# Kernel tuning notes

Hardware: AMD Instinct MI355X
Metric: run time of the kernel (lower is better)

Reference implementation:

```python
import jax, jax.numpy as jnp
import numpy as np
import math

NL = 2
ENC = 64

def _ln(x, g, b):
    m = x.mean(-1, keepdims=True)
    v = ((x - m) ** 2).mean(-1, keepdims=True)
    return (x - m) * jax.lax.rsqrt(v + 1e-5) * g + b

def _sinu(vals):
    half = ENC // 2
    freq = jnp.exp(jnp.arange(half, dtype=vals.dtype) * (-math.log(10000.0) / half))
    a = vals[..., None] * freq
    return jnp.concatenate([jnp.sin(a), jnp.cos(a)], -1)

def _ssm(x, ng, nb, piw, pib, pw, pb, ig, ib):
    # SSMBlock with LinearAttention core: x + proj_out(LN(silu(z)*sigmoid(gate)))
    h = _ln(x, ng, nb)
    zi = h @ piw + pib
    z, gate = jnp.split(zi, 2, axis=-1)
    u = _ln(jax.nn.silu(z) * jax.nn.sigmoid(gate), ig, ib)
    return x + u @ pw + pb

def _fwd(s, attn_maps, km, se_w1, se_b1, se_w2, se_b2,
         f_ng, f_nb, f_piw, f_pib, f_pow, f_pob, f_ig, f_ib,
         b_ng, b_nb, b_piw, b_pib, b_pow, b_pob, b_ig, b_ib,
         mrg_w, mrg_b, nrm_g, nrm_b,
         ffn_ng, ffn_nb, ffn_w1, ffn_b1, ffn_w2, ffn_b2, H, W):
    B, K, D = s.shape
    w = attn_maps / (attn_maps.sum(-1, keepdims=True) + 1e-8)  # [B,K,N]
    gy = jnp.arange(H, dtype=s.dtype) / max(H - 1, 1)
    gx = jnp.arange(W, dtype=s.dtype) / max(W - 1, 1)
    grid_y = jnp.repeat(gy, W)  # [N], meshgrid-ij flattened
    grid_x = jnp.tile(gx, H)
    cy = (w * grid_y).sum(-1)  # [B,K]
    cx = (w * grid_x).sum(-1)
    spread = jnp.sqrt((w * ((grid_y - cy[..., None]) ** 2 + (grid_x - cx[..., None]) ** 2)).sum(-1))
    enc = jnp.concatenate([_sinu(cy), _sinu(cx), spread[..., None]], -1)  # [B,K,129]
    s = s + jax.nn.gelu(enc @ se_w1 + se_b1, approximate=False) @ se_w2 + se_b2
    # spatial order: identical every layer since attn_maps is fixed
    order = jnp.argsort(cy * W + cx, axis=-1)  # [B,K]
    rv = jnp.argsort(order, axis=-1)           # inverse permutation
    for i in range(NL):
        r = s
        so = jnp.take_along_axis(s, order[..., None], axis=1)
        f = _ssm(so, f_ng[i], f_nb[i], f_piw[i], f_pib[i], f_pow[i], f_pob[i], f_ig[i], f_ib[i])
        bb = jnp.flip(_ssm(jnp.flip(so, 1), b_ng[i], b_nb[i], b_piw[i], b_pib[i], b_pow[i], b_pob[i], b_ig[i], b_ib[i]), 1)
        m = jnp.concatenate([f, bb], -1) @ mrg_w[i] + mrg_b[i]
        s = _ln(r + jnp.take_along_axis(m, rv[..., None], axis=1), nrm_g[i], nrm_b[i])
        h = _ln(s, ffn_ng[i], ffn_nb[i])
        s = s + jax.nn.gelu(h @ ffn_w1[i] + ffn_b1[i], approximate=False) @ ffn_w2[i] + ffn_b2[i]
        s = s * km[..., None]
    return s

def setup_inputs() -> dict:
    B, K, D, DI, H, W = 32, 256, 512, 1024, 64, 64
    N = H * W
    ks = iter(jax.random.split(jax.random.key(0), 64))
    def g(shape, sc=0.02):
        return jax.random.normal(next(ks), shape, dtype=jnp.float32) * sc
    inp = {
        's': jax.random.normal(next(ks), (B, K, D), dtype=jnp.float32),
        'attn_maps': jax.random.uniform(next(ks), (B, K, N), dtype=jnp.float32),
        'km': jnp.ones((B, K), jnp.float32),
        'se_w1': g((2 * ENC + 1, D)), 'se_b1': jnp.zeros((D,), jnp.float32),
        'se_w2': g((D, D)), 'se_b2': jnp.zeros((D,), jnp.float32),
    }
    for p in ('f', 'b'):
        inp[p + '_ng'] = jnp.ones((NL, D), jnp.float32)
        inp[p + '_nb'] = jnp.zeros((NL, D), jnp.float32)
        inp[p + '_piw'] = g((NL, D, 2 * DI))
        inp[p + '_pib'] = jnp.zeros((NL, 2 * DI), jnp.float32)
        inp[p + '_pow'] = g((NL, DI, D))
        inp[p + '_pob'] = jnp.zeros((NL, D), jnp.float32)
        inp[p + '_ig'] = jnp.ones((NL, DI), jnp.float32)
        inp[p + '_ib'] = jnp.zeros((NL, DI), jnp.float32)
    inp['mrg_w'] = g((NL, 2 * D, D)); inp['mrg_b'] = jnp.zeros((NL, D), jnp.float32)
    inp['nrm_g'] = jnp.ones((NL, D), jnp.float32); inp['nrm_b'] = jnp.zeros((NL, D), jnp.float32)
    inp['ffn_ng'] = jnp.ones((NL, D), jnp.float32); inp['ffn_nb'] = jnp.zeros((NL, D), jnp.float32)
    inp['ffn_w1'] = g((NL, D, 4 * D)); inp['ffn_b1'] = jnp.zeros((NL, 4 * D), jnp.float32)
    inp['ffn_w2'] = g((NL, 4 * D, D)); inp['ffn_b2'] = jnp.zeros((NL, D), jnp.float32)
    inp['H'] = H
    inp['W'] = W
    return inp

def reference(s, attn_maps, km, se_w1, se_b1, se_w2, se_b2,
              f_ng, f_nb, f_piw, f_pib, f_pow, f_pob, f_ig, f_ib,
              b_ng, b_nb, b_piw, b_pib, b_pow, b_pob, b_ig, b_ib,
              mrg_w, mrg_b, nrm_g, nrm_b,
              ffn_ng, ffn_nb, ffn_w1, ffn_b1, ffn_w2, ffn_b2, H, W):
    return _fwd(s, attn_maps, km, se_w1, se_b1, se_w2, se_b2,
                f_ng, f_nb, f_piw, f_pib, f_pow, f_pob, f_ig, f_ib,
                b_ng, b_nb, b_piw, b_pib, b_pow, b_pob, b_ig, b_ib,
                mrg_w, mrg_b, nrm_g, nrm_b,
                ffn_ng, ffn_nb, ffn_w1, ffn_b1, ffn_w2, ffn_b2, H, W)
```

## Files before the change

kernel.cpp:

```cpp
#include <hip/hip_runtime.h>
#include <cstdint>
#include <cstddef>


typedef unsigned short u16;
typedef __bf16 bf16x8 __attribute__((ext_vector_type(8)));
typedef float f32x4 __attribute__((ext_vector_type(4)));

#define MROWS 8192

__device__ __forceinline__ u16 f2bf(float f){
  unsigned u = __float_as_uint(f);
  u += 0x7FFFu + ((u >> 16) & 1u);
  return (u16)(u >> 16);
}
__device__ __forceinline__ float bf2f(u16 v){
  return __uint_as_float((unsigned)v << 16);
}

__device__ __forceinline__ float wred64(float v){
#pragma unroll
  for (int o = 32; o > 0; o >>= 1) v += __shfl_xor(v, o, 64);
  return v;
}

#define GLD16(gp, lp) __builtin_amdgcn_global_load_lds( \
    (const __attribute__((address_space(1))) unsigned int*)(gp), \
    (__attribute__((address_space(3))) unsigned int*)(lp), 16, 0, 0)

struct TDesc { const float* src; u16* dst; int R, Kpad, C, zgate, nbx, base; };
struct TPack { TDesc d[16]; };

__global__ __launch_bounds__(256) void transpose_all(TPack p){
  int bid = blockIdx.x;
  TDesc dd = p.d[0];
#pragma unroll
  for (int i = 1; i < 16; ++i) if (bid >= p.d[i].base) dd = p.d[i];
  int lb = bid - dd.base;
  int bx = lb % dd.nbx, by = lb / dd.nbx;

  __shared__ float tile[32][33];
  int n0 = bx << 5, k0 = by << 5;
  int tx = threadIdx.x & 31, ty = threadIdx.x >> 5;
#pragma unroll
  for (int i = 0; i < 32; i += 8){
    int k = k0 + ty + i, n = n0 + tx;
    int oc = n;
    if (dd.zgate){ int g = n >> 5, sl = n & 31;
      oc = (sl < 16) ? (g << 4) + sl : (dd.C >> 1) + (g << 4) + sl - 16; }
    tile[ty + i][tx] = (k < dd.R) ? dd.src[(size_t)k * dd.C + oc] : 0.f;
  }
  __syncthreads();
#pragma unroll
  for (int i = 0; i < 32; i += 8){
    int n = n0 + ty + i, k = k0 + tx;
    dd.dst[(size_t)n * dd.Kpad + k] = f2bf(tile[tx][ty + i]);
  }
}

__global__ __launch_bounds__(256) void stats_enc(
    const float* __restrict__ attn, u16* __restrict__ enc){
  int row = blockIdx.x;
  const float4* a4 = (const float4*)(attn + (size_t)row * 4096);
  int t = threadIdx.x;
  const float inv63 = 1.0f / 63.0f;
  float s0 = 0, sy = 0, sx = 0, sy2 = 0, sx2 = 0;
#pragma unroll
  for (int i = 0; i < 4; ++i){
    int c = t + 256 * i;
    float4 v = a4[c];
    int n = 4 * c;
#pragma unroll
    for (int e = 0; e < 4; ++e){
      float av = (&v.x)[e];
      int nn = n + e;
      float gy = (float)(nn >> 6) * inv63;
      float gx = (float)(nn & 63) * inv63;
      s0 += av; sy += av * gy; sx += av * gx;
      sy2 += av * gy * gy; sx2 += av * gx * gx;
    }
  }
  s0 = wred64(s0); sy = wred64(sy); sx = wred64(sx);
  sy2 = wred64(sy2); sx2 = wred64(sx2);
  __shared__ float red[4][5];
  __shared__ float outv[3];
  int wv = t >> 6, lane = t & 63;
  if (lane == 0){ red[wv][0]=s0; red[wv][1]=sy; red[wv][2]=sx; red[wv][3]=sy2; red[wv][4]=sx2; }
  __syncthreads();
  if (t == 0){
    float S=0, Ay=0, Ax=0, Ay2=0, Ax2=0;
    for (int w = 0; w < 4; ++w){ S+=red[w][0]; Ay+=red[w][1]; Ax+=red[w][2]; Ay2+=red[w][3]; Ax2+=red[w][4]; }
    float denom = S + 1e-8f;
    float cy = Ay / denom, cx = Ax / denom;
    float sp2 = (Ay2 - 2.f*cy*Ay + cy*cy*S + Ax2 - 2.f*cx*Ax + cx*cx*S) / denom;
    outv[0] = cy; outv[1] = cx; outv[2] = sqrtf(fmaxf(sp2, 0.f));
  }
  __syncthreads();
  if (t < 192){
    float cy = outv[0], cx = outv[1];
    float val = 0.f;
    if (t < 128){
      int j = t & 31;
      float fr = expf(-0.28782313662425572f * (float)j);
      float base = (t < 64) ? cy : cx;
      float ang = base * fr;
      val = ((t >> 5) & 1) ? cosf(ang) : sinf(ang);
    } else if (t == 128) val = outv[2];
    enc[(size_t)row * 192 + t] = f2bf(val);
  }
}

__global__ __launch_bounds__(256) void ln_dual(
    const float* __restrict__ x,
    const float* __restrict__ g1, const float* __restrict__ b1,
    const float* __restrict__ g2, const float* __restrict__ b2,
    u16* __restrict__ o1, u16* __restrict__ o2){
  int row = blockIdx.x * 4 + (threadIdx.x >> 6);
  int lane = threadIdx.x & 63, c = lane * 8;
  const float* xr = x + (size_t)row * 512 + c;
  float v[8];
  *(float4*)(v) = *(const float4*)(xr); *(float4*)(v+4) = *(const float4*)(xr+4);
  float s = 0.f;
#pragma unroll
  for (int j = 0; j < 8; ++j) s += v[j];
  float m = wred64(s) * (1.f/512.f);
  float q = 0.f;
#pragma unroll
  for (int j = 0; j < 8; ++j){ float d = v[j]-m; q += d*d; }
  float rstd = rsqrtf(wred64(q)*(1.f/512.f) + 1e-5f);
  float G1[8],B1[8],G2[8],B2[8];
  *(float4*)(G1)=*(const float4*)(g1+c); *(float4*)(G1+4)=*(const float4*)(g1+c+4);
  *(float4*)(B1)=*(const float4*)(b1+c); *(float4*)(B1+4)=*(const float4*)(b1+c+4);
  *(float4*)(G2)=*(const float4*)(g2+c); *(float4*)(G2+4)=*(const float4*)(g2+c+4);
  *(float4*)(B2)=*(const float4*)(b2+c); *(float4*)(B2+4)=*(const float4*)(b2+c+4);
  u16 u1[8] __attribute__((aligned(16)));
  u16 u2[8] __attribute__((aligned(16)));
#pragma unroll
  for (int j = 0; j < 8; ++j){
    float nv = (v[j]-m)*rstd;
    u1[j] = f2bf(nv*G1[j]+B1[j]);
    u2[j] = f2bf(nv*G2[j]+B2[j]);
  }
  *(uint4*)(o1 + (size_t)row*512 + c) = *(const uint4*)u1;
  *(uint4*)(o2 + (size_t)row*512 + c) = *(const uint4*)u2;
}

__global__ __launch_bounds__(256) void ln1024(
    const u16* __restrict__ x, const float* __restrict__ g,
    const float* __restrict__ b, u16* __restrict__ o){
  int row = blockIdx.x * 4 + (threadIdx.x >> 6);
  int lane = threadIdx.x & 63, c = lane * 16;
  const u16* xr = x + (size_t)row * 1024 + c;
  u16 raw[16] __attribute__((aligned(16)));
  *(uint4*)(raw)     = *(const uint4*)(xr);
  *(uint4*)(raw + 8) = *(const uint4*)(xr + 8);
  float v[16];
#pragma unroll
  for (int j = 0; j < 16; ++j) v[j] = bf2f(raw[j]);
  float s = 0.f;
#pragma unroll
  for (int j = 0; j < 16; ++j) s += v[j];
  float m = wred64(s) * (1.f/1024.f);
  float q = 0.f;
#pragma unroll
  for (int j = 0; j < 16; ++j){ float d = v[j]-m; q += d*d; }
  float rstd = rsqrtf(wred64(q)*(1.f/1024.f) + 1e-5f);
  float G[16], B[16];
#pragma unroll
  for (int i = 0; i < 4; ++i){
    *(float4*)(G + 4*i) = *(const float4*)(g + c + 4*i);
    *(float4*)(B + 4*i) = *(const float4*)(b + c + 4*i);
  }
  u16 u[16] __attribute__((aligned(16)));
#pragma unroll
  for (int j = 0; j < 16; ++j) u[j] = f2bf((v[j]-m)*rstd*G[j] + B[j]);
  *(uint4*)(o + (size_t)row*1024 + c)     = *(const uint4*)(u);
  *(uint4*)(o + (size_t)row*1024 + c + 8) = *(const uint4*)(u + 8);
}

__global__ __launch_bounds__(256) void ln_double(
    const float* __restrict__ x,
    const float* __restrict__ ng, const float* __restrict__ nb,
    const float* __restrict__ fg, const float* __restrict__ fbv,
    float* __restrict__ s1, u16* __restrict__ h2){
  int row = blockIdx.x * 4 + (threadIdx.x >> 6);
  int lane = threadIdx.x & 63, c = lane * 8;
  const float* xr = x + (size_t)row * 512 + c;
  float v[8];
  *(float4*)(v) = *(const float4*)(xr); *(float4*)(v+4) = *(const float4*)(xr+4);
  float s = 0.f;
#pragma unroll
  for (int j = 0; j < 8; ++j) s += v[j];
  float m = wred64(s) * (1.f/512.f);
  float q = 0.f;
#pragma unroll
  for (int j = 0; j < 8; ++j){ float d = v[j]-m; q += d*d; }
  float rstd = rsqrtf(wred64(q)*(1.f/512.f) + 1e-5f);
  float NG[8],NB[8],FG[8],FB[8];
  *(float4*)(NG)=*(const float4*)(ng+c); *(float4*)(NG+4)=*(const float4*)(ng+c+4);
  *(float4*)(NB)=*(const float4*)(nb+c); *(float4*)(NB+4)=*(const float4*)(nb+c+4);
  *(float4*)(FG)=*(const float4*)(fg+c); *(float4*)(FG+4)=*(const float4*)(fg+c+4);
  *(float4*)(FB)=*(const float4*)(fbv+c);*(float4*)(FB+4)=*(const float4*)(fbv+c+4);
  float w[8];
#pragma unroll
  for (int j = 0; j < 8; ++j) w[j] = (v[j]-m)*rstd*NG[j] + NB[j];
  *(float4*)(s1 + (size_t)row*512 + c)   = *(const float4*)(w);
  *(float4*)(s1 + (size_t)row*512 + c+4) = *(const float4*)(w+4);
  float s2 = 0.f;
#pragma unroll
  for (int j = 0; j < 8; ++j) s2 += w[j];
  float m2 = wred64(s2) * (1.f/512.f);
  float q2 = 0.f;
#pragma unroll
  for (int j = 0; j < 8; ++j){ float d = w[j]-m2; q2 += d*d; }
  float rstd2 = rsqrtf(wred64(q2)*(1.f/512.f) + 1e-5f);
  u16 u[8] __attribute__((aligned(16)));
#pragma unroll
  for (int j = 0; j < 8; ++j) u[j] = f2bf((w[j]-m2)*rstd2*FG[j] + FB[j]);
  *(uint4*)(h2 + (size_t)row*512 + c) = *(const uint4*)u;
}

template<int EPI, int BM>
__global__ __launch_bounds__(256, 2) void gemm_bt(
    const u16* __restrict__ A, const u16* __restrict__ BT,
    const float* __restrict__ bias, const float* __restrict__ res,
    float* __restrict__ outF, u16* __restrict__ outB,
    const float* __restrict__ km,
    int K, int N, int ldo, int coloff){
  constexpr int MR = BM / 32;
  __shared__ u16 Asm[BM * 64];
  __shared__ u16 Bsm[128 * 64];
  const int tid = threadIdx.x, wv = tid >> 6, lane = tid & 63;
  const int m0 = blockIdx.y * BM, n0 = blockIdx.x << 7;
  const int wr = wv >> 1, wc = wv & 1;

  const int rowin = lane >> 3;
  const int ksrc = ((16 * (lane & 7)) ^ (rowin << 4)) >> 1;
  const int rA = wv * (BM / 4) + rowin;
  const int rB = (wv << 5) + rowin;
  const u16* gA = A + (size_t)(m0 + rA) * K + ksrc;
  const u16* gB = BT + (size_t)(n0 + rB) * K + ksrc;
  u16* ldsA = Asm + wv * (BM / 4) * 64;
  u16* ldsB = Bsm + (wv << 11);

  f32x4 acc[MR][4] = {};
  const int cbase = 16 * (lane >> 4);
  const int swz = (lane & 7) << 4;

  for (int kt = 0; kt < K; kt += 64){
#pragma unroll
    for (int it = 0; it < BM / 32; ++it)
      GLD16(gA + (size_t)it * 8 * K + kt, ldsA + it * 512);
#pragma unroll
    for (int it = 0; it < 4; ++it)
      GLD16(gB + (size_t)it * 8 * K + kt, ldsB + it * 512);
    __syncthreads();
#pragma unroll
    for (int ks = 0; ks < 64; ks += 32){
      const int cs = ((2 * ks + cbase) ^ swz) >> 1;
      bf16x8 af[MR], bfr[4];
#pragma unroll
      for (int m = 0; m < MR; ++m)
        af[m] = *reinterpret_cast<const bf16x8*>(&Asm[(wr*(BM/2) + m*16 + (lane & 15)) * 64 + cs]);
#pragma unroll
      for (int n = 0; n < 4; ++n)
        bfr[n] = *reinterpret_cast<const bf16x8*>(&Bsm[(wc*64 + n*16 + (lane & 15)) * 64 + cs]);
#pragma unroll
      for (int m = 0; m < MR; ++m)
#pragma unroll
        for (int n = 0; n < 4; ++n)
          acc[m][n] = __builtin_amdgcn_mfma_f32_16x16x32_bf16(af[m], bfr[n], acc[m][n], 0, 0, 0);
    }
    __syncthreads();
  }

  const int lr = (lane >> 4) << 2, lc = lane & 15;
#pragma unroll
  for (int m = 0; m < MR; ++m){
    const int grow0 = m0 + wr * (BM/2) + m * 16 + lr;
    if constexpr (EPI == 3){
#pragma unroll
      for (int n = 0; n < 4; n += 2){
        const int zc = n0 + wc * 64 + n * 16 + lc;
        const int bi = ((zc >> 5) << 4) + lc;
        const float bz = bias[bi], bg = bias[(N >> 1) + bi];
        const int ucol = ((n0 + wc * 64) >> 1) + (n << 3) + lc;
#pragma unroll
        for (int r = 0; r < 4; ++r){
          float z = acc[m][n][r] + bz;
          float g = acc[m][n + 1][r] + bg;
          outB[(size_t)(grow0 + r) * ldo + ucol] =
              f2bf((z / (1.f + expf(-z))) * (1.f / (1.f + expf(-g))));
        }
      }
    } else {
#pragma unroll
      for (int n = 0; n < 4; ++n){
        const int col = n0 + wc * 64 + n * 16 + lc;
        const float bv = bias[col];
#pragma unroll
        for (int r = 0; r < 4; ++r){
          const int grow = grow0 + r;
          float v = acc[m][n][r] + bv;
          if constexpr (EPI == 0){
            outB[(size_t)grow * ldo + col] = f2bf(0.5f * v * (1.f + erff(v * 0.70710678118654752f)));
          } else if constexpr (EPI == 1){
            outF[(size_t)grow * ldo + col] = v + res[(size_t)grow * N + col];
          } else if constexpr (EPI == 2){
            outF[(size_t)grow * ldo + col] = (v + res[(size_t)grow * N + col]) * km[grow];
          } else {
            outB[(size_t)grow * ldo + coloff + col] = f2bf(v + res[(size_t)grow * N + col]);
          }
        }
      }
    }
  }
}

extern "C" void kernel_launch(void* const* d_in, const int* in_sizes, int n_in,
                              void* d_out, int out_size, void* d_ws, size_t ws_size,
                              hipStream_t stream){
  (void)in_sizes; (void)n_in; (void)out_size; (void)ws_size;
  const float* s_in   = (const float*)d_in[0];
  const float* attn   = (const float*)d_in[1];
  const float* km     = (const float*)d_in[2];
  const float* se_w1  = (const float*)d_in[3];
  const float* se_b1  = (const float*)d_in[4];
  const float* se_w2  = (const float*)d_in[5];
  const float* se_b2  = (const float*)d_in[6];
  const float* png[2] = {(const float*)d_in[7],  (const float*)d_in[15]};
  const float* pnb[2] = {(const float*)d_in[8],  (const float*)d_in[16]};
  const float* ppiw[2]= {(const float*)d_in[9],  (const float*)d_in[17]};
  const float* ppib[2]= {(const float*)d_in[10], (const float*)d_in[18]};
  const float* ppow[2]= {(const float*)d_in[11], (const float*)d_in[19]};
  const float* ppob[2]= {(const float*)d_in[12], (const float*)d_in[20]};
  const float* pig[2] = {(const float*)d_in[13], (const float*)d_in[21]};
  const float* pibt[2]= {(const float*)d_in[14], (const float*)d_in[22]};
  const float* mrg_w  = (const float*)d_in[23];
  const float* mrg_b  = (const float*)d_in[24];
  const float* nrm_g  = (const float*)d_in[25];
  const float* nrm_b  = (const float*)d_in[26];
  const float* ffn_ng = (const float*)d_in[27];
  const float* ffn_nb = (const float*)d_in[28];
  const float* ffn_w1 = (const float*)d_in[29];
  const float* ffn_b1 = (const float*)d_in[30];
  const float* ffn_w2 = (const float*)d_in[31];
  const float* ffn_b2 = (const float*)d_in[32];
  float* out = (float*)d_out;

  char* ws = (char*)d_ws;
  size_t off = 0;
  auto alloc = [&](size_t bytes)->char*{
    char* p = ws + off; off += (bytes + 255) & ~(size_t)255; return p; };

  u16* w_sew1 = (u16*)alloc(512 * 192 * 2);
  u16* w_sew2 = (u16*)alloc(512 * 512 * 2);
  u16* w_piw[2][2]; u16* w_pow[2][2];
  for (int d = 0; d < 2; ++d)
    for (int i = 0; i < 2; ++i){
      w_piw[d][i] = (u16*)alloc(2048 * 512 * 2);
      w_pow[d][i] = (u16*)alloc(512 * 1024 * 2);
    }
  u16* w_mrg[2]; u16* w_ffn1[2]; u16* w_ffn2[2];
  for (int i = 0; i < 2; ++i){
    w_mrg[i]  = (u16*)alloc(512 * 1024 * 2);
    w_ffn1[i] = (u16*)alloc(2048 * 512 * 2);
    w_ffn2[i] = (u16*)alloc(512 * 2048 * 2);
  }
  u16*   enc  = (u16*)alloc((size_t)MROWS * 192 * 2);
  u16*   t1h2 = (u16*)alloc((size_t)MROWS * 512 * 2);
  float* sc   = (float*)alloc((size_t)MROWS * 512 * 4);
  u16*   hf   = (u16*)alloc((size_t)MROWS * 512 * 2);
  u16*   hb   = (u16*)alloc((size_t)MROWS * 512 * 2);
  char*  big  = alloc((size_t)MROWS * 1024 * 4);
  u16*   upre = (u16*)big;
  float* r2   = (float*)big;
  u16*   t2   = (u16*)big;
  u16*   ubf  = (u16*)alloc((size_t)MROWS * 1024 * 2);
  u16*   fbuf = (u16*)alloc((size_t)MROWS * 1024 * 2);
  float* s1   = (float*)alloc((size_t)MROWS * 512 * 4);

  TPack pk; int base = 0, di = 0;
  auto push = [&](const float* src, u16* dst, int R, int Kpad, int C, int zg){
    TDesc& t = pk.d[di++];
    t.src = src; t.dst = dst; t.R = R; t.Kpad = Kpad; t.C = C; t.zgate = zg;
    t.nbx = C / 32; t.base = base;
    base += (C / 32) * (Kpad / 32);
  };
  push(se_w1, w_sew1, 129, 192, 512, 0);
  push(se_w2, w_sew2, 512, 512, 512, 0);
  for (int d = 0; d < 2; ++d)
    for (int i = 0; i < 2; ++i){
      push(ppiw[d] + (size_t)i*512*2048, w_piw[d][i], 512, 512, 2048, 1);
      push(ppow[d] + (size_t)i*1024*512, w_pow[d][i], 1024, 1024, 512, 0);
    }
  for (int i = 0; i < 2; ++i){
    push(mrg_w  + (size_t)i*1024*512, w_mrg[i],  1024, 1024, 512, 0);
    push(ffn_w1 + (size_t)i*512*2048, w_ffn1[i], 512, 512, 2048, 0);
    push(ffn_w2 + (size_t)i*2048*512, w_ffn2[i], 2048, 2048, 512, 0);
  }
  transpose_all<<<base, 256, 0, stream>>>(pk);

  stats_enc<<<MROWS, 256, 0, stream>>>(attn, enc);
  gemm_bt<0,64><<<dim3(4, 128), 256, 0, stream>>>(enc,  w_sew1, se_b1, nullptr, nullptr, t1h2, nullptr, 192, 512, 512, 0);
  gemm_bt<1,64><<<dim3(4, 128), 256, 0, stream>>>(t1h2, w_sew2, se_b2, s_in,    sc,      nullptr, nullptr, 512, 512, 512, 0);

  for (int i = 0; i < 2; ++i){
    ln_dual<<<MROWS/4, 256, 0, stream>>>(sc, png[0]+i*512, pnb[0]+i*512,
                                         png[1]+i*512, pnb[1]+i*512, hf, hb);
    for (int d = 0; d < 2; ++d){
      const u16* h = d ? hb : hf;
      gemm_bt<3,128><<<dim3(16, 64), 256, 0, stream>>>(h, w_piw[d][i], ppib[d]+(size_t)i*2048,
          nullptr, nullptr, upre, nullptr, 512, 2048, 1024, 0);
      ln1024<<<MROWS/4, 256, 0, stream>>>(upre, pig[d]+i*1024, pibt[d]+i*1024, ubf);
      gemm_bt<4,64><<<dim3(4, 128), 256, 0, stream>>>(ubf, w_pow[d][i], ppob[d]+i*512,
          sc, nullptr, fbuf, nullptr, 1024, 512, 1024, d*512);
    }
    gemm_bt<1,64><<<dim3(4, 128), 256, 0, stream>>>(fbuf, w_mrg[i], mrg_b+i*512,
        sc, r2, nullptr, nullptr, 1024, 512, 512, 0);
    ln_double<<<MROWS/4, 256, 0, stream>>>(r2, nrm_g+i*512, nrm_b+i*512,
        ffn_ng+i*512, ffn_nb+i*512, s1, t1h2);
    gemm_bt<0,128><<<dim3(16, 64), 256, 0, stream>>>(t1h2, w_ffn1[i], ffn_b1+i*2048,
        nullptr, nullptr, t2, nullptr, 512, 2048, 2048, 0);
    gemm_bt<2,64><<<dim3(4, 128), 256, 0, stream>>>(t2, w_ffn2[i], ffn_b2+i*512,
        s1, (i == 1 ? out : sc), nullptr, km, 2048, 512, 512, 0);
  }
}
```

Before: 832.2 us.

## Batch forward/backward SSM GEMMs into single launches and store residuals in bf16

Forward and backward SSM branches are stacked into one 2×MROWS activation buffer. Their in-projection GEMM, the inner LayerNorm and the out-projection GEMM each run as a single launch, with per-row selection of weights, biases and LN parameters. The merge output r2 and the post-norm residual s1 are now stored as bf16 instead of fp32, which halves their traffic but adds rounding error on the residual path. BM=64 GEMMs also get a higher min-blocks-per-CU launch bound, which limits register use to allow more occupancy.

```diff
diff --git a/kernel.cpp b/kernel.cpp
--- a/kernel.cpp
+++ b/kernel.cpp
@@ -146,10 +146,14 @@
 }
 
 __global__ __launch_bounds__(256) void ln1024(
-    const u16* __restrict__ x, const float* __restrict__ g,
-    const float* __restrict__ b, u16* __restrict__ o){
+    const u16* __restrict__ x,
+    const float* __restrict__ gf, const float* __restrict__ bfp,
+    const float* __restrict__ gb, const float* __restrict__ bbp,
+    u16* __restrict__ o){
   int row = blockIdx.x * 4 + (threadIdx.x >> 6);
   int lane = threadIdx.x & 63, c = lane * 16;
+  const float* g = (row >> 13) ? gb : gf;
+  const float* b = (row >> 13) ? bbp : bfp;
   const u16* xr = x + (size_t)row * 1024 + c;
   u16 raw[16] __attribute__((aligned(16)));
   *(uint4*)(raw)     = *(const uint4*)(xr);
@@ -179,15 +183,18 @@
 }
 
 __global__ __launch_bounds__(256) void ln_double(
-    const float* __restrict__ x,
+    const u16* __restrict__ x,
     const float* __restrict__ ng, const float* __restrict__ nb,
     const float* __restrict__ fg, const float* __restrict__ fbv,
-    float* __restrict__ s1, u16* __restrict__ h2){
+    u16* __restrict__ s1, u16* __restrict__ h2){
   int row = blockIdx.x * 4 + (threadIdx.x >> 6);
   int lane = threadIdx.x & 63, c = lane * 8;
-  const float* xr = x + (size_t)row * 512 + c;
+  const u16* xr = x + (size_t)row * 512 + c;
+  u16 raw[8] __attribute__((aligned(16)));
+  *(uint4*)(raw) = *(const uint4*)(xr);
   float v[8];
-  *(float4*)(v) = *(const float4*)(xr); *(float4*)(v+4) = *(const float4*)(xr+4);
+#pragma unroll
+  for (int j = 0; j < 8; ++j) v[j] = bf2f(raw[j]);
   float s = 0.f;
 #pragma unroll
   for (int j = 0; j < 8; ++j) s += v[j];
@@ -204,8 +211,10 @@
   float w[8];
 #pragma unroll
   for (int j = 0; j < 8; ++j) w[j] = (v[j]-m)*rstd*NG[j] + NB[j];
-  *(float4*)(s1 + (size_t)row*512 + c)   = *(const float4*)(w);
-  *(float4*)(s1 + (size_t)row*512 + c+4) = *(const float4*)(w+4);
+  u16 us[8] __attribute__((aligned(16)));
+#pragma unroll
+  for (int j = 0; j < 8; ++j) us[j] = f2bf(w[j]);
+  *(uint4*)(s1 + (size_t)row*512 + c) = *(const uint4*)us;
   float s2 = 0.f;
 #pragma unroll
   for (int j = 0; j < 8; ++j) s2 += w[j];
@@ -221,18 +230,22 @@
 }
 
 template<int EPI, int BM>
-__global__ __launch_bounds__(256, 2) void gemm_bt(
-    const u16* __restrict__ A, const u16* __restrict__ BT,
-    const float* __restrict__ bias, const float* __restrict__ res,
+__global__ __launch_bounds__(256, (BM == 64) ? 4 : 2) void gemm_bt(
+    const u16* __restrict__ A,
+    const u16* __restrict__ BT0, const u16* __restrict__ BT1,
+    const float* __restrict__ bias0, const float* __restrict__ bias1,
+    const void* __restrict__ res,
     float* __restrict__ outF, u16* __restrict__ outB,
     const float* __restrict__ km,
-    int K, int N, int ldo, int coloff){
+    int K, int N, int ldo){
   constexpr int MR = BM / 32;
   __shared__ u16 Asm[BM * 64];
   __shared__ u16 Bsm[128 * 64];
   const int tid = threadIdx.x, wv = tid >> 6, lane = tid & 63;
   const int m0 = blockIdx.y * BM, n0 = blockIdx.x << 7;
   const int wr = wv >> 1, wc = wv & 1;
+  const u16* BT = (m0 < MROWS) ? BT0 : BT1;
+  const float* bias = (m0 < MROWS) ? bias0 : bias1;
 
   const int rowin = lane >> 3;
   const int ksrc = ((16 * (lane & 7)) ^ (rowin << 4)) >> 1;
@@ -305,11 +318,15 @@
           if constexpr (EPI == 0){
             outB[(size_t)grow * ldo + col] = f2bf(0.5f * v * (1.f + erff(v * 0.70710678118654752f)));
           } else if constexpr (EPI == 1){
-            outF[(size_t)grow * ldo + col] = v + res[(size_t)grow * N + col];
+            outF[(size_t)grow * ldo + col] = v + ((const float*)res)[(size_t)grow * N + col];
           } else if constexpr (EPI == 2){
-            outF[(size_t)grow * ldo + col] = (v + res[(size_t)grow * N + col]) * km[grow];
+            outF[(size_t)grow * ldo + col] =
+                (v + bf2f(((const u16*)res)[(size_t)grow * N + col])) * km[grow];
           } else {
-            outB[(size_t)grow * ldo + coloff + col] = f2bf(v + res[(size_t)grow * N + col]);
+            const int rowout = grow & (MROWS - 1);
+            const int coloff = (grow >> 13) << 9;
+            outB[(size_t)rowout * ldo + coloff + col] =
+                f2bf(v + ((const float*)res)[(size_t)rowout * N + col]);
           }
         }
       }
@@ -370,15 +387,14 @@
   u16*   enc  = (u16*)alloc((size_t)MROWS * 192 * 2);
   u16*   t1h2 = (u16*)alloc((size_t)MROWS * 512 * 2);
   float* sc   = (float*)alloc((size_t)MROWS * 512 * 4);
-  u16*   hf   = (u16*)alloc((size_t)MROWS * 512 * 2);
-  u16*   hb   = (u16*)alloc((size_t)MROWS * 512 * 2);
-  char*  big  = alloc((size_t)MROWS * 1024 * 4);
+  u16*   hcat = (u16*)alloc((size_t)2 * MROWS * 512 * 2);
+  char*  big  = alloc((size_t)MROWS * 2048 * 2);
   u16*   upre = (u16*)big;
-  float* r2   = (float*)big;
+  u16*   r2   = (u16*)big;
   u16*   t2   = (u16*)big;
-  u16*   ubf  = (u16*)alloc((size_t)MROWS * 1024 * 2);
+  u16*   ubf  = (u16*)alloc((size_t)2 * MROWS * 1024 * 2);
   u16*   fbuf = (u16*)alloc((size_t)MROWS * 1024 * 2);
-  float* s1   = (float*)alloc((size_t)MROWS * 512 * 4);
+  u16*   s1   = (u16*)alloc((size_t)MROWS * 512 * 2);
 
   TPack pk; int base = 0, di = 0;
   auto push = [&](const float* src, u16* dst, int R, int Kpad, int C, int zg){
@@ -402,27 +418,32 @@
   transpose_all<<<base, 256, 0, stream>>>(pk);
 
   stats_enc<<<MROWS, 256, 0, stream>>>(attn, enc);
-  gemm_bt<0,64><<<dim3(4, 128), 256, 0, stream>>>(enc,  w_sew1, se_b1, nullptr, nullptr, t1h2, nullptr, 192, 512, 512, 0);
-  gemm_bt<1,64><<<dim3(4, 128), 256, 0, stream>>>(t1h2, w_sew2, se_b2, s_in,    sc,      nullptr, nullptr, 512, 512, 512, 0);
+  gemm_bt<0,64><<<dim3(4, 128), 256, 0, stream>>>(enc, w_sew1, w_sew1, se_b1, se_b1,
+      nullptr, nullptr, t1h2, nullptr, 192, 512, 512);
+  gemm_bt<1,64><<<dim3(4, 128), 256, 0, stream>>>(t1h2, w_sew2, w_sew2, se_b2, se_b2,
+      s_in, sc, nullptr, nullptr, 512, 512, 512);
 
   for (int i = 0; i < 2; ++i){
     ln_dual<<<MROWS/4, 256, 0, stream>>>(sc, png[0]+i*512, pnb[0]+i*512,
-                                         png[1]+i*512, pnb[1]+i*512, hf, hb);
-    for (int d = 0; d < 2; ++d){
-      const u16* h = d ? hb : hf;
-      gemm_bt<3,128><<<dim3(16, 64), 256, 0, stream>>>(h, w_piw[d][i], ppib[d]+(size_t)i*2048,
-          nullptr, nullptr, upre, nullptr, 512, 2048, 1024, 0);
-      ln1024<<<MROWS/4, 256, 0, stream>>>(upre, pig[d]+i*1024, pibt[d]+i*1024, ubf);
-      gemm_bt<4,64><<<dim3(4, 128), 256, 0, stream>>>(ubf, w_pow[d][i], ppob[d]+i*512,
-          sc, nullptr, fbuf, nullptr, 1024, 512, 1024, d*512);
-    }
-    gemm_bt<1,64><<<dim3(4, 128), 256, 0, stream>>>(fbuf, w_mrg[i], mrg_b+i*512,
-        sc, r2, nullptr, nullptr, 1024, 512, 512, 0);
+        png[1]+i*512, pnb[1]+i*512, hcat, hcat + (size_t)MROWS*512);
+    gemm_bt<3,128><<<dim3(16, 128), 256, 0, stream>>>(hcat,
+        w_piw[0][i], w_piw[1][i], ppib[0]+(size_t)i*2048, ppib[1]+(size_t)i*2048,
+        nullptr, nullptr, upre, nullptr, 512, 2048, 1024);
+    ln1024<<<(2*MROWS)/4, 256, 0, stream>>>(upre,
+        pig[0]+i*1024, pibt[0]+i*1024, pig[1]+i*1024, pibt[1]+i*1024, ubf);
+    gemm_bt<4,64><<<dim3(4, 256), 256, 0, stream>>>(ubf,
+        w_pow[0][i], w_pow[1][i], ppob[0]+i*512, ppob[1]+i*512,
+        sc, nullptr, fbuf, nullptr, 1024, 512, 1024);
+    gemm_bt<4,64><<<dim3(4, 128), 256, 0, stream>>>(fbuf,
+        w_mrg[i], w_mrg[i], mrg_b+i*512, mrg_b+i*512,
+        sc, nullptr, r2, nullptr, 1024, 512, 512);
     ln_double<<<MROWS/4, 256, 0, stream>>>(r2, nrm_g+i*512, nrm_b+i*512,
         ffn_ng+i*512, ffn_nb+i*512, s1, t1h2);
-    gemm_bt<0,128><<<dim3(16, 64), 256, 0, stream>>>(t1h2, w_ffn1[i], ffn_b1+i*2048,
-        nullptr, nullptr, t2, nullptr, 512, 2048, 2048, 0);
-    gemm_bt<2,64><<<dim3(4, 128), 256, 0, stream>>>(t2, w_ffn2[i], ffn_b2+i*512,
-        s1, (i == 1 ? out : sc), nullptr, km, 2048, 512, 512, 0);
-  }
-}
+    gemm_bt<0,128><<<dim3(16, 64), 256, 0, stream>>>(t1h2,
+        w_ffn1[i], w_ffn1[i], ffn_b1+i*2048, ffn_b1+i*2048,
+        nullptr, nullptr, t2, nullptr, 512, 2048, 2048);
+    gemm_bt<2,64><<<dim3(4, 128), 256, 0, stream>>>(t2,
+        w_ffn2[i], w_ffn2[i], ffn_b2+i*512, ffn_b2+i*512,
+        s1, (i == 1 ? out : sc), nullptr, km, 2048, 512, 512);
+  }
+}
```

Result: faster. 751.9 us (median of 2 runs) (-9.7%).
